# Kernel optimization log

Measured on AMD Instinct MI355X. Metric: run time of the kernel, lower is better.

Reference implementation:

```python
import jax, jax.numpy as jnp
import numpy as np

D_MODEL = 1024
BLOCK_SIZE = 2048


def setup_inputs() -> dict:
    key = jax.random.key(0)
    ks = jax.random.split(key, 9)
    B, T, C = 4, 2048, D_MODEL
    s = 1.0 / np.sqrt(C)
    return {
        "x": jax.random.normal(ks[0], (B, T, C), dtype=jnp.float32),
        "Wq": jax.random.normal(ks[1], (C, C), dtype=jnp.float32) * s,
        "bq": jnp.zeros((C,), dtype=jnp.float32),
        "Wk": jax.random.normal(ks[2], (C, C), dtype=jnp.float32) * s,
        "bk": jnp.zeros((C,), dtype=jnp.float32),
        "Wv": jax.random.normal(ks[3], (C, C), dtype=jnp.float32) * s,
        "bv": jnp.zeros((C,), dtype=jnp.float32),
        "Wo": jax.random.normal(ks[4], (C, C), dtype=jnp.float32) * s,
        "bo": jnp.zeros((C,), dtype=jnp.float32),
    }


def reference(x, Wq, bq, Wk, bk, Wv, bv, Wo, bo):
    B, T, C = x.shape
    q = x @ Wq + bq
    k = x @ Wk + bk
    v = x @ Wv + bv
    # NOTE: original module never splits heads; attention is over full d_model
    score = jnp.einsum("btc,bsc->bts", q, k) / jnp.sqrt(jnp.asarray(C, x.dtype))
    causal = jnp.tril(jnp.ones((T, T), dtype=bool))
    score = jnp.where(causal, score, jnp.asarray(-jnp.inf, x.dtype))
    probs = jax.nn.softmax(score, axis=-1)
    out = jnp.einsum("bts,bsc->btc", probs, v)
    return out @ Wo + bo
```

## Files before the change

### kernel.cpp

```cpp
#include <hip/hip_runtime.h>
#include <hip/hip_bf16.h>
#include <stdint.h>


typedef __attribute__((ext_vector_type(8))) __bf16 bf16x8;
typedef __attribute__((ext_vector_type(4))) __bf16 bf16x4;
typedef __attribute__((ext_vector_type(4))) float f32x4;

#define MFMA16(A, B, C) __builtin_amdgcn_mfma_f32_16x16x32_bf16(A, B, C, 0, 0, 0)
#define BAR() asm volatile("s_barrier" ::: "memory")

#define T_SEQ 2048
#define D_MOD 1024

static __device__ __forceinline__ void gload_lds16(const void* g, void* l) {
  __builtin_amdgcn_global_load_lds(
      (const __attribute__((address_space(1))) void*)g,
      (__attribute__((address_space(3))) void*)l, 16, 0, 0);
}

__global__ void cvt_bf16_kernel(const float* __restrict__ in,
                                __bf16* __restrict__ out, int n8) {
  int i = blockIdx.x * blockDim.x + threadIdx.x;
  if (i < n8) {
    const float4* p = (const float4*)(in + (size_t)i * 8);
    float4 a = p[0], b = p[1];
    bf16x8 o;
    o[0] = (__bf16)a.x; o[1] = (__bf16)a.y; o[2] = (__bf16)a.z; o[3] = (__bf16)a.w;
    o[4] = (__bf16)b.x; o[5] = (__bf16)b.y; o[6] = (__bf16)b.z; o[7] = (__bf16)b.w;
    *(bf16x8*)(out + (size_t)i * 8) = o;
  }
}

__global__ void transpose_cvt4_kernel(const float* __restrict__ Wq,
                                      const float* __restrict__ Wk,
                                      const float* __restrict__ Wv,
                                      const float* __restrict__ Wo,
                                      __bf16* __restrict__ Wqkvt,
                                      __bf16* __restrict__ Wot) {
  __shared__ float tile[32][33];
  const int z = blockIdx.z;
  const float* W = (z == 0) ? Wq : (z == 1) ? Wk : (z == 2) ? Wv : Wo;
  __bf16* Wt = (z < 3) ? (Wqkvt + (size_t)z * 1024 * 1024) : Wot;
  int tx = threadIdx.x, ty = threadIdx.y;
  int bx = blockIdx.x * 32, by = blockIdx.y * 32;
#pragma unroll
  for (int i = 0; i < 4; i++)
    tile[ty + 8 * i][tx] = W[(size_t)(by + ty + 8 * i) * D_MOD + bx + tx];
  __syncthreads();
#pragma unroll
  for (int i = 0; i < 4; i++)
    Wt[(size_t)(bx + ty + 8 * i) * D_MOD + by + tx] = (__bf16)tile[tx][ty + 8 * i];
}

__global__ __launch_bounds__(512, 2) void qkv384_kernel(
    const __bf16* __restrict__ A, const __bf16* __restrict__ Bt,
    const float* __restrict__ bq, const float* __restrict__ bk,
    const float* __restrict__ bv, __bf16* __restrict__ Qo,
    __bf16* __restrict__ Ko, __bf16* __restrict__ Vto) {
  constexpr int NT = 16;
  __shared__ __align__(16) char lds[131072];
#define ABUF(p) (lds + (p) * 16384)
#define BBUF(p) (lds + 32768 + (p) * 49152)

  const int tid = threadIdx.x;
  const int w = tid >> 6, l = tid & 63;
  const int wr = w >> 2, wc = w & 3;
  const int cpx = gridDim.x >> 3;
  const int swz = ((int)blockIdx.x & 7) * cpx + ((int)blockIdx.x >> 3);
  const int bm = (swz >> 3) * 128;
  const int bn = (swz & 7) * 384;

  const int cswz = (l & 3) ^ ((l >> 3) & 3);
  const int rlo = l & 15;
  const int xsw = (((l >> 4) ^ ((l >> 1) & 3)) << 4);

#define STAGE_A(t, p)                                                     \
  {                                                                       \
    const __bf16* g = A + (size_t)(bm + w * 16 + (l >> 2)) * 1024 +       \
                      (t) * 64 + cswz * 8;                                \
    char* d = ABUF(p) + w * 1024 + l * 16;                                \
    gload_lds16(g, d);                                                    \
    gload_lds16(g + 32, d + 8192);                                        \
  }
#define STAGE_B(t, p, gch)                                                \
  {                                                                       \
    const __bf16* g = Bt +                                                \
        (size_t)(bn + ((gch) * 8 + w) * 16 + (l >> 2)) * 1024 +           \
        (t) * 64 + cswz * 8;                                              \
    char* d = BBUF(p) + ((gch) * 8 + w) * 1024 + l * 16;                  \
    gload_lds16(g, d);                                                    \
    gload_lds16(g + 32, d + 24576);                                       \
  }
#define LDA_FRAG(p, i, kk)                                        \
  (*(const bf16x8*)(ABUF(p) + (kk) * 8192 +                       \
                    (wr * 64 + (i) * 16 + rlo) * 64 + xsw))
#define LDB_FRAG(p, gch, n, kk)                                   \
  (*(const bf16x8*)(BBUF(p) + (kk) * 24576 +                      \
                    (wc * 96 + (gch) * 32 + (n) * 16 + rlo) * 64 + xsw))

  f32x4 acc[4][6] = {};
  bf16x8 a_c[4][2], a_n[4][2], b0_c[2][2], b0_n[2][2], b1f[2][2], b2f[2][2];

  STAGE_A(0, 0);
  STAGE_B(0, 0, 0); STAGE_B(0, 0, 1); STAGE_B(0, 0, 2);
  STAGE_A(1, 1);
  STAGE_B(1, 1, 0); STAGE_B(1, 1, 1); STAGE_B(1, 1, 2);
  asm volatile("s_waitcnt vmcnt(8)" ::: "memory");
  BAR();
#pragma unroll
  for (int i = 0; i < 4; i++) {
    a_c[i][0] = LDA_FRAG(0, i, 0);
    a_c[i][1] = LDA_FRAG(0, i, 1);
  }
#pragma unroll
  for (int n = 0; n < 2; n++) {
    b0_c[n][0] = LDB_FRAG(0, 0, n, 0);
    b0_c[n][1] = LDB_FRAG(0, 0, n, 1);
  }

  for (int t = 0; t < NT; ++t) {
    const int p = t & 1;
#pragma unroll
    for (int n = 0; n < 2; n++) {
      b1f[n][0] = LDB_FRAG(p, 1, n, 0);
      b1f[n][1] = LDB_FRAG(p, 1, n, 1);
    }
    __builtin_amdgcn_s_setprio(1);
#pragma unroll
    for (int i = 0; i < 4; i++)
#pragma unroll
      for (int n = 0; n < 2; n++) {
        acc[i][n] = MFMA16(a_c[i][0], b0_c[n][0], acc[i][n]);
        acc[i][n] = MFMA16(a_c[i][1], b0_c[n][1], acc[i][n]);
      }
    __builtin_amdgcn_s_setprio(0);
    BAR();
#pragma unroll
    for (int n = 0; n < 2; n++) {
      b2f[n][0] = LDB_FRAG(p, 2, n, 0);
      b2f[n][1] = LDB_FRAG(p, 2, n, 1);
    }
    if (t + 2 < NT) STAGE_A(t + 2, p);
    __builtin_amdgcn_s_setprio(1);
#pragma unroll
    for (int i = 0; i < 4; i++)
#pragma unroll
      for (int n = 0; n < 2; n++) {
        acc[i][2 + n] = MFMA16(a_c[i][0], b1f[n][0], acc[i][2 + n]);
        acc[i][2 + n] = MFMA16(a_c[i][1], b1f[n][1], acc[i][2 + n]);
      }
    __builtin_amdgcn_s_setprio(0);
    if (t + 2 < NT) asm volatile("s_waitcnt vmcnt(2)" ::: "memory");
    else asm volatile("s_waitcnt vmcnt(0)" ::: "memory");
    BAR();
    if (t + 1 < NT) {
#pragma unroll
      for (int i = 0; i < 4; i++) {
        a_n[i][0] = LDA_FRAG(p ^ 1, i, 0);
        a_n[i][1] = LDA_FRAG(p ^ 1, i, 1);
      }
#pragma unroll
      for (int n = 0; n < 2; n++) {
        b0_n[n][0] = LDB_FRAG(p ^ 1, 0, n, 0);
        b0_n[n][1] = LDB_FRAG(p ^ 1, 0, n, 1);
      }
    }
    if (t + 2 < NT) {
      STAGE_B(t + 2, p, 0); STAGE_B(t + 2, p, 1); STAGE_B(t + 2, p, 2);
    }
    __builtin_amdgcn_s_setprio(1);
#pragma unroll
    for (int i = 0; i < 4; i++)
#pragma unroll
      for (int n = 0; n < 2; n++) {
        acc[i][4 + n] = MFMA16(a_c[i][0], b2f[n][0], acc[i][4 + n]);
        acc[i][4 + n] = MFMA16(a_c[i][1], b2f[n][1], acc[i][4 + n]);
      }
    __builtin_amdgcn_s_setprio(0);
    BAR();
    if (t + 1 < NT) {
#pragma unroll
      for (int i = 0; i < 4; i++) {
        a_c[i][0] = a_n[i][0];
        a_c[i][1] = a_n[i][1];
      }
#pragma unroll
      for (int n = 0; n < 2; n++) {
        b0_c[n][0] = b0_n[n][0];
        b0_c[n][1] = b0_n[n][1];
      }
    }
  }

  const int l4 = (l >> 4) * 4;
#pragma unroll
  for (int gch = 0; gch < 3; gch++)
#pragma unroll
    for (int n = 0; n < 2; n++) {
      const int cbase = bn + wc * 96 + gch * 32 + n * 16;
      const int seg = cbase >> 10;
      const int lcol = (cbase & 1023) + rlo;
      const int an = gch * 2 + n;
      if (seg < 2) {
        const float* bs = seg ? bk : bq;
        __bf16* os = seg ? Ko : Qo;
        const float bvv = bs[lcol];
#pragma unroll
        for (int i = 0; i < 4; i++) {
          const int rowb = bm + wr * 64 + i * 16 + l4;
#pragma unroll
          for (int r = 0; r < 4; r++)
            os[(size_t)(rowb + r) * D_MOD + lcol] =
                (__bf16)(acc[i][an][r] + bvv);
        }
      } else {
        const float bvv = bv[lcol];
#pragma unroll
        for (int i = 0; i < 4; i++) {
          const int rowb = bm + wr * 64 + i * 16 + l4;
          const int z = rowb >> 11, tt = rowb & 2047;
          bf16x4 pk;
#pragma unroll
          for (int r = 0; r < 4; r++) pk[r] = (__bf16)(acc[i][an][r] + bvv);
          *(bf16x4*)(Vto + (size_t)z * (D_MOD * T_SEQ) +
                     (size_t)lcol * T_SEQ + tt) = pk;
        }
      }
    }
#undef ABUF
#undef BBUF
#undef STAGE_A
#undef STAGE_B
#undef LDA_FRAG
#undef LDB_FRAG
}

template <int MG, int NG>
static __device__ __forceinline__ void mfma_quad(f32x4 (&acc)[8][4],
                                                 const bf16x8 (&aR)[4][2],
                                                 const bf16x8 (&bR)[2][2]) {
#pragma unroll
  for (int i = 0; i < 4; i++)
#pragma unroll
    for (int n = 0; n < 2; n++)
#pragma unroll
      for (int kk = 0; kk < 2; kk++)
        acc[MG * 4 + i][NG * 2 + n] =
            MFMA16(aR[i][kk], bR[n][kk], acc[MG * 4 + i][NG * 2 + n]);
}

__global__ __launch_bounds__(512, 2) void qk_kernel(
    const __bf16* __restrict__ A, const __bf16* __restrict__ Bt,
    float* __restrict__ So, size_t bsA, size_t bsB, size_t bsC) {
  constexpr int NT = 16;
  __shared__ __align__(16) char lds[131072];
#define ABUF(p, h) (lds + ((p) * 2 + (h)) * 16384)
#define BBUF(p, h) (lds + 65536 + ((p) * 2 + (h)) * 16384)

  const int tid = threadIdx.x;
  const int w = tid >> 6, l = tid & 63;
  const int wr = w >> 2, wc = w & 3;
  int x = (int)blockIdx.x;
  int ti = 0;
  while (x >= ti + 1) { x -= ti + 1; ++ti; }
  const int tj = x;
  const int bm = ti * 256, bn = tj * 256;
  const int z = blockIdx.z;
  A += (size_t)z * bsA;
  Bt += (size_t)z * bsB;

  const int grow = l >> 2;
  const int cswz = (l & 3) ^ ((l >> 3) & 3);
  const int rlo = l & 15;
  const int xsw = (((l >> 4) ^ ((l >> 1) & 3)) << 4);

#define STAGE_A(t, h)                                                       \
  {                                                                         \
    const __bf16* g = A + (size_t)(bm + (h) * 128 + w * 16 + grow) * 1024 + \
                      (t) * 64 + cswz * 8;                                  \
    char* d = ABUF((t) & 1, h) + w * 1024 + l * 16;                         \
    gload_lds16(g, d);                                                      \
    gload_lds16(g + 32, d + 8192);                                          \
  }
#define STAGE_B(t, h)                                                       \
  {                                                                         \
    const __bf16* g = Bt + (size_t)(bn + (h) * 128 + w * 16 + grow) * 1024 +\
                      (t) * 64 + cswz * 8;                                  \
    char* d = BBUF((t) & 1, h) + w * 1024 + l * 16;                         \
    gload_lds16(g, d);                                                      \
    gload_lds16(g + 32, d + 8192);                                          \
  }
#define LDA_FRAG(p, g, i, kk)                                     \
  (*(const bf16x8*)(ABUF(p, wr) + (kk) * 8192 +                   \
                    ((g) * 64 + (i) * 16 + rlo) * 64 + xsw))
#define LDB_FRAG(p, g, n, kk)                                     \
  (*(const bf16x8*)(BBUF(p, (wc >> 1)) + (kk) * 8192 +            \
                    ((wc & 1) * 64 + (g) * 32 + (n) * 16 + rlo) * 64 + xsw))

  f32x4 acc[8][4] = {};
  STAGE_A(0, 0); STAGE_A(0, 1);
  STAGE_B(0, 0); STAGE_B(0, 1);
  STAGE_A(1, 0); STAGE_A(1, 1);
  asm volatile("s_waitcnt vmcnt(4)" ::: "memory");
  BAR();

  for (int t = 0; t < NT; ++t) {
    const int p = t & 1;
    bf16x8 a[4][2], b[2][2];
#pragma unroll
    for (int i = 0; i < 4; i++) {
      a[i][0] = LDA_FRAG(p, 0, i, 0);
      a[i][1] = LDA_FRAG(p, 0, i, 1);
    }
#pragma unroll
    for (int n = 0; n < 2; n++) {
      b[n][0] = LDB_FRAG(p, 0, n, 0);
      b[n][1] = LDB_FRAG(p, 0, n, 1);
    }
    if (t + 1 < NT) STAGE_B(t + 1, 0);
    BAR();
    __builtin_amdgcn_s_setprio(1);
    mfma_quad<0, 0>(acc, a, b);
    __builtin_amdgcn_s_setprio(0);
    BAR();
    bf16x8 b2[2][2];
#pragma unroll
    for (int n = 0; n < 2; n++) {
      b2[n][0] = LDB_FRAG(p, 1, n, 0);
      b2[n][1] = LDB_FRAG(p, 1, n, 1);
    }
    if (t + 1 < NT) STAGE_B(t + 1, 1);
    BAR();
    __builtin_amdgcn_s_setprio(1);
    mfma_quad<0, 1>(acc, a, b2);
    __builtin_amdgcn_s_setprio(0);
    BAR();
#pragma unroll
    for (int i = 0; i < 4; i++) {
      a[i][0] = LDA_FRAG(p, 1, i, 0);
      a[i][1] = LDA_FRAG(p, 1, i, 1);
    }
    BAR();
    __builtin_amdgcn_s_setprio(1);
    mfma_quad<1, 1>(acc, a, b2);
    __builtin_amdgcn_s_setprio(0);
    BAR();
#pragma unroll
    for (int n = 0; n < 2; n++) {
      b[n][0] = LDB_FRAG(p, 0, n, 0);
      b[n][1] = LDB_FRAG(p, 0, n, 1);
    }
    if (t + 2 < NT) {
      STAGE_A(t + 2, 0); STAGE_A(t + 2, 1);
      BAR();
      __builtin_amdgcn_s_setprio(1);
      mfma_quad<1, 0>(acc, a, b);
      __builtin_amdgcn_s_setprio(0);
      asm volatile("s_waitcnt vmcnt(4)" ::: "memory");
      BAR();
    } else {
      BAR();
      __builtin_amdgcn_s_setprio(1);
      mfma_quad<1, 0>(acc, a, b);
      __builtin_amdgcn_s_setprio(0);
      asm volatile("s_waitcnt vmcnt(0)" ::: "memory");
      BAR();
    }
  }

  float* os = So + (size_t)z * bsC;
#pragma unroll
  for (int n4 = 0; n4 < 4; n4++) {
    int col = bn + wc * 64 + n4 * 16 + rlo;
#pragma unroll
    for (int mi = 0; mi < 8; mi++) {
      int rowb = bm + wr * 128 + mi * 16 + (l >> 4) * 4;
#pragma unroll
      for (int r = 0; r < 4; r++) {
        int row = rowb + r;
        float v = acc[mi][n4][r] * 0.03125f;
        if (col > row) v = -1e30f;
        os[(size_t)row * T_SEQ + col] = v;
      }
    }
  }
#undef ABUF
#undef BBUF
#undef STAGE_A
#undef STAGE_B
#undef LDA_FRAG
#undef LDB_FRAG
}

__global__ __launch_bounds__(512, 2) void pv_kernel(
    const __bf16* __restrict__ Ap, const __bf16* __restrict__ Btp,
    __bf16* __restrict__ Op, size_t bsA, size_t bsB, size_t bsC) {
  __shared__ __align__(16) char lds[98304];
#define ABUF(p3) (lds + (p3) * 16384)
#define BBUF(p3) (lds + 49152 + (p3) * 16384)

  const int tid = threadIdx.x;
  const int w = tid >> 6, l = tid & 63;
  const int wr = w >> 2, wc = w & 3;
  const int pid = (int)blockIdx.x >> 3;
  const int bn = ((int)blockIdx.x & 7) * 128;
  const int z = blockIdx.z;
  const __bf16* A = Ap + (size_t)z * bsA;
  const __bf16* Bt = Btp + (size_t)z * bsB;
  __bf16* O = Op + (size_t)z * bsC;

  const int grow = w * 16 + (l >> 2);
  const int cswz = (l & 3) ^ ((l >> 3) & 3);
  const int rlo = l & 15;
  const int xsw = (((l >> 4) ^ ((l >> 1) & 3)) << 4);

#define PSTAGE_A(t, p3)                                                      \
  {                                                                          \
    const __bf16* g = A + (size_t)(bm + grow) * 4096 + (t) * 64 + cswz * 8;  \
    char* d = ABUF(p3) + w * 1024 + l * 16;                                  \
    gload_lds16(g, d);                                                       \
    gload_lds16(g + 32, d + 8192);                                           \
  }
#define PSTAGE_B(t, p3)                                                      \
  {                                                                          \
    const __bf16* g = Bt + (size_t)(bn + grow) * 2048 + (t) * 64 + cswz * 8; \
    char* d = BBUF(p3) + w * 1024 + l * 16;                                  \
    gload_lds16(g, d);                                                       \
    gload_lds16(g + 32, d + 8192);                                           \
  }
#define PLDA(p3, i, kk)                                           \
  (*(const bf16x8*)(ABUF(p3) + (kk) * 8192 +                      \
                    (wr * 64 + (i) * 16 + rlo) * 64 + xsw))
#define PLDB(p3, n, kk)                                           \
  (*(const bf16x8*)(BBUF(p3) + (kk) * 8192 +                      \
                    (wc * 32 + (n) * 16 + rlo) * 64 + xsw))

#pragma unroll
  for (int seg = 0; seg < 2; ++seg) {
    const int i = seg ? (15 - pid) : pid;
    const int bm = i * 128;
    const int NT = (i + 1) * 2;
    f32x4 acc[4][2] = {};

    PSTAGE_A(0, 0); PSTAGE_B(0, 0);
    if (NT > 1) { PSTAGE_A(1, 1); PSTAGE_B(1, 1); }
    asm volatile("s_waitcnt vmcnt(4)" ::: "memory");
    BAR();

    int p = 0, pn2 = 2;
    for (int t = 0; t < NT; ++t) {
      bf16x8 af[4][2], bfv[2][2];
#pragma unroll
      for (int m = 0; m < 4; m++) {
        af[m][0] = PLDA(p, m, 0);
        af[m][1] = PLDA(p, m, 1);
      }
#pragma unroll
      for (int n = 0; n < 2; n++) {
        bfv[n][0] = PLDB(p, n, 0);
        bfv[n][1] = PLDB(p, n, 1);
      }
      if (t + 2 < NT) { PSTAGE_A(t + 2, pn2); PSTAGE_B(t + 2, pn2); }
      BAR();
      __builtin_amdgcn_s_setprio(1);
#pragma unroll
      for (int m = 0; m < 4; m++)
#pragma unroll
        for (int n = 0; n < 2; n++) {
          acc[m][n] = MFMA16(af[m][0], bfv[n][0], acc[m][n]);
          acc[m][n] = MFMA16(af[m][1], bfv[n][1], acc[m][n]);
        }
      __builtin_amdgcn_s_setprio(0);
      if (t + 2 < NT) asm volatile("s_waitcnt vmcnt(4)" ::: "memory");
      else asm volatile("s_waitcnt vmcnt(0)" ::: "memory");
      BAR();
      p = (p + 1 == 3) ? 0 : p + 1;
      pn2 = (pn2 + 1 == 3) ? 0 : pn2 + 1;
    }

#pragma unroll
    for (int n = 0; n < 2; n++) {
      int col = bn + wc * 32 + n * 16 + rlo;
#pragma unroll
      for (int m = 0; m < 4; m++) {
        int rowb = bm + wr * 64 + m * 16 + (l >> 4) * 4;
#pragma unroll
        for (int r = 0; r < 4; r++)
          O[(size_t)(rowb + r) * D_MOD + col] = (__bf16)acc[m][n][r];
      }
    }
    BAR();
  }
#undef ABUF
#undef BBUF
#undef PSTAGE_A
#undef PSTAGE_B
#undef PLDA
#undef PLDB
}

__global__ __launch_bounds__(512, 2) void oproj_kernel(
    const __bf16* __restrict__ A, const __bf16* __restrict__ Bt,
    const float* __restrict__ b0, float* __restrict__ o0) {
  constexpr int NT = 16;
  __shared__ __align__(16) char lds[147456];
#define ABUF(p3) (lds + (p3) * 16384)
#define BBUF(p3) (lds + 49152 + (p3) * 32768)

  const int tid = threadIdx.x;
  const int w = tid >> 6, l = tid & 63;
  const int wr = w >> 2, wc = w & 3;
  const int cpx = gridDim.x >> 3;
  const int swz = ((int)blockIdx.x & 7) * cpx + ((int)blockIdx.x >> 3);
  const int bm = (swz >> 2) * 128, bn = (swz & 3) * 256;

  const int grow = w * 16 + (l >> 2);
  const int cswz = (l & 3) ^ ((l >> 3) & 3);
  const int rlo = l & 15;
  const int xsw = (((l >> 4) ^ ((l >> 1) & 3)) << 4);

#define STAGE_A(t, p3)                                                       \
  {                                                                          \
    const __bf16* g = A + (size_t)(bm + grow) * 1024 + (t) * 64 + cswz * 8;  \
    char* d = ABUF(p3) + w * 1024 + l * 16;                                  \
    gload_lds16(g, d);                                                       \
    gload_lds16(g + 32, d + 8192);                                           \
  }
#define STAGE_B(t, p3)                                                       \
  {                                                                          \
    const __bf16* g = Bt + (size_t)(bn + grow) * 1024 + (t) * 64 + cswz * 8; \
    char* d = BBUF(p3) + w * 1024 + l * 16;                                  \
    gload_lds16(g, d);                                                       \
    gload_lds16(g + 32, d + 16384);                                          \
    const __bf16* g2 = g + (size_t)128 * 1024;                               \
    gload_lds16(g2, d + 8192);                                               \
    gload_lds16(g2 + 32, d + 8192 + 16384);                                  \
  }
#define LDA_FRAG(p3, i, kk)                                       \
  (*(const bf16x8*)(ABUF(p3) + (kk) * 8192 +                      \
                    (wr * 64 + (i) * 16 + rlo) * 64 + xsw))
#define LDB_FRAG(p3, n, kk)                                       \
  (*(const bf16x8*)(BBUF(p3) + (kk) * 16384 +                     \
                    (wc * 64 + (n) * 16 + rlo) * 64 + xsw))

  f32x4 acc[4][4] = {};
  STAGE_A(0, 0); STAGE_B(0, 0);
  STAGE_A(1, 1); STAGE_B(1, 1);
  asm volatile("s_waitcnt vmcnt(6)" ::: "memory");
  BAR();

  int p = 0, pn2 = 2;
  for (int t = 0; t < NT; ++t) {
    bf16x8 af[4][2], bf01[2][2], bf23[2][2];
#pragma unroll
    for (int i = 0; i < 4; i++) {
      af[i][0] = LDA_FRAG(p, i, 0);
      af[i][1] = LDA_FRAG(p, i, 1);
    }
#pragma unroll
    for (int n = 0; n < 2; n++) {
      bf01[n][0] = LDB_FRAG(p, n, 0);
      bf01[n][1] = LDB_FRAG(p, n, 1);
    }
    if (t + 2 < NT) STAGE_A(t + 2, pn2);
    BAR();
    __builtin_amdgcn_s_setprio(1);
#pragma unroll
    for (int i = 0; i < 4; i++)
#pragma unroll
      for (int n = 0; n < 2; n++) {
        acc[i][n] = MFMA16(af[i][0], bf01[n][0], acc[i][n]);
        acc[i][n] = MFMA16(af[i][1], bf01[n][1], acc[i][n]);
      }
    __builtin_amdgcn_s_setprio(0);
    BAR();
#pragma unroll
    for (int n = 0; n < 2; n++) {
      bf23[n][0] = LDB_FRAG(p, n + 2, 0);
      bf23[n][1] = LDB_FRAG(p, n + 2, 1);
    }
    if (t + 2 < NT) STAGE_B(t + 2, pn2);
    BAR();
    __builtin_amdgcn_s_setprio(1);
#pragma unroll
    for (int i = 0; i < 4; i++)
#pragma unroll
      for (int n = 0; n < 2; n++) {
        acc[i][n + 2] = MFMA16(af[i][0], bf23[n][0], acc[i][n + 2]);
        acc[i][n + 2] = MFMA16(af[i][1], bf23[n][1], acc[i][n + 2]);
      }
    __builtin_amdgcn_s_setprio(0);
    if (t + 2 < NT) {
      asm volatile("s_waitcnt vmcnt(6)" ::: "memory");
    } else {
      asm volatile("s_waitcnt vmcnt(0)" ::: "memory");
    }
    BAR();
    p = (p + 1 == 3) ? 0 : p + 1;
    pn2 = (pn2 + 1 == 3) ? 0 : pn2 + 1;
  }

#pragma unroll
  for (int n = 0; n < 4; n++) {
    int col = bn + wc * 64 + n * 16 + rlo;
    float bvv = b0[col];
#pragma unroll
    for (int m = 0; m < 4; m++) {
      int rowb = bm + wr * 64 + m * 16 + (l >> 4) * 4;
#pragma unroll
      for (int r = 0; r < 4; r++)
        o0[(size_t)(rowb + r) * D_MOD + col] = acc[m][n][r] + bvv;
    }
  }
#undef ABUF
#undef BBUF
#undef STAGE_A
#undef STAGE_B
#undef LDA_FRAG
#undef LDB_FRAG
}

__global__ __launch_bounds__(256) void softmax_kernel(float* __restrict__ S,
                                                      size_t bstride) {
  const int t = blockIdx.x, b = blockIdx.y;
  float* Srow = S + (size_t)b * bstride + (size_t)t * T_SEQ;
  __bf16* Prow = (__bf16*)Srow;
  const int L = ((t + 1) + 127) & ~127;
  const int tid = threadIdx.x;
  const int base = tid * 8;
  const bool act = base < L;
  float v[8];
  float m = -1e30f;
  if (act) {
    float4 a = *(const float4*)(Srow + base);
    float4 c = *(const float4*)(Srow + base + 4);
    v[0] = a.x; v[1] = a.y; v[2] = a.z; v[3] = a.w;
    v[4] = c.x; v[5] = c.y; v[6] = c.z; v[7] = c.w;
#pragma unroll
    for (int j = 0; j < 8; j++) m = fmaxf(m, v[j]);
  }
#pragma unroll
  for (int off = 1; off < 64; off <<= 1) m = fmaxf(m, __shfl_xor(m, off));
  __shared__ float redm[4], reds[4];
  const int wave = tid >> 6, lane = tid & 63;
  if (lane == 0) redm[wave] = m;
  __syncthreads();
  m = fmaxf(fmaxf(redm[0], redm[1]), fmaxf(redm[2], redm[3]));
  float p[8];
  float s = 0.f;
  if (act) {
#pragma unroll
    for (int j = 0; j < 8; j++) {
      p[j] = __expf(v[j] - m);
      s += p[j];
    }
  }
#pragma unroll
  for (int off = 1; off < 64; off <<= 1) s += __shfl_xor(s, off);
  if (lane == 0) reds[wave] = s;
  __syncthreads();
  const float inv = 1.0f / (reds[0] + reds[1] + reds[2] + reds[3]);
  if (act) {
    bf16x8 o;
#pragma unroll
    for (int j = 0; j < 8; j++) o[j] = (__bf16)(p[j] * inv);
    *(bf16x8*)(Prow + base) = o;
  }
}

extern "C" void kernel_launch(void* const* d_in, const int* in_sizes, int n_in,
                              void* d_out, int out_size, void* d_ws,
                              size_t ws_size, hipStream_t stream) {
  const float* x = (const float*)d_in[0];
  const float* Wq = (const float*)d_in[1];
  const float* bq = (const float*)d_in[2];
  const float* Wk = (const float*)d_in[3];
  const float* bk = (const float*)d_in[4];
  const float* Wv = (const float*)d_in[5];
  const float* bv = (const float*)d_in[6];
  const float* Wo = (const float*)d_in[7];
  const float* bo = (const float*)d_in[8];

  char* ws = (char*)d_ws;
  const size_t MB = 1u << 20;
  const size_t TC = (size_t)T_SEQ * D_MOD;
  const size_t TT = (size_t)T_SEQ * T_SEQ;
  __bf16* xb    = (__bf16*)(ws);
  __bf16* Wqkvt = (__bf16*)(ws + 16 * MB);
  __bf16* Wot   = (__bf16*)(ws + 22 * MB);
  __bf16* Qb    = (__bf16*)(ws + 24 * MB);
  __bf16* Kb    = (__bf16*)(ws + 40 * MB);
  __bf16* Vtb   = (__bf16*)(ws + 56 * MB);

  cvt_bf16_kernel<<<4096, 256, 0, stream>>>(x, xb, 8192 * D_MOD / 8);
  transpose_cvt4_kernel<<<dim3(32, 32, 4), dim3(32, 8), 0, stream>>>(
      Wq, Wk, Wv, Wo, Wqkvt, Wot);
  qkv384_kernel<<<512, 512, 0, stream>>>(xb, Wqkvt, bq, bk, bv, Qb, Kb, Vtb);

  const bool batched = ws_size >= 137 * MB;
  if (batched) {
    float* S = (float*)(ws + 72 * MB);
    __bf16* AO = Qb;
    qk_kernel<<<dim3(36, 1, 4), 512, 0, stream>>>(Qb, Kb, S, TC, TC, TT);
    softmax_kernel<<<dim3(T_SEQ, 4), 256, 0, stream>>>(S, TT);
    pv_kernel<<<dim3(64, 1, 4), 512, 0, stream>>>((const __bf16*)S, Vtb, AO,
                                                  TT * 2, TC, TC);
    oproj_kernel<<<256, 512, 0, stream>>>(AO, Wot, bo, (float*)d_out);
  } else {
    float* S = (float*)(ws);
    __bf16* AO = Qb;
    for (int b = 0; b < 4; ++b) {
      qk_kernel<<<dim3(36, 1, 1), 512, 0, stream>>>(Qb + b * TC, Kb + b * TC,
                                                    S, 0, 0, 0);
      softmax_kernel<<<dim3(T_SEQ, 1), 256, 0, stream>>>(S, 0);
      pv_kernel<<<dim3(64, 1, 1), 512, 0, stream>>>(
          (const __bf16*)S, Vtb + b * TC, AO + b * TC, 0, 0, 0);
    }
    oproj_kernel<<<256, 512, 0, stream>>>(AO, Wot, bo, (float*)d_out);
  }
}
```

Measured before the change: 170.4 us.

## Replace 128x384 QKV GEMM tile with 128x256 tile and simpler pipeline

Replaces the QKV projection kernel's 128x384 output tile (K-step 64, 128KB LDS) with a 128x256 tile (K-step 32, 48KB LDS), launched on 768 blocks instead of 512. The main loop becomes a simpler double-buffered loop with one fragment load phase and one MFMA phase per step, and the staggered register prefetch is dropped. The aim is to cut LDS use so more blocks fit per CU and to balance work across CUs. The trade-off is less data reuse per tile, twice as many K iterations, and two barriers per step with less overlap of loads and math.

```diff
diff --git a/kernel.cpp b/kernel.cpp
--- a/kernel.cpp
+++ b/kernel.cpp
@@ -53,187 +53,116 @@
     Wt[(size_t)(bx + ty + 8 * i) * D_MOD + by + tx] = (__bf16)tile[tx][ty + 8 * i];
 }
 
-__global__ __launch_bounds__(512, 2) void qkv384_kernel(
+__global__ __launch_bounds__(512, 2) void qkv256_kernel(
     const __bf16* __restrict__ A, const __bf16* __restrict__ Bt,
     const float* __restrict__ bq, const float* __restrict__ bk,
     const float* __restrict__ bv, __bf16* __restrict__ Qo,
     __bf16* __restrict__ Ko, __bf16* __restrict__ Vto) {
-  constexpr int NT = 16;
-  __shared__ __align__(16) char lds[131072];
-#define ABUF(p) (lds + (p) * 16384)
-#define BBUF(p) (lds + 32768 + (p) * 49152)
+  constexpr int NT = 32;
+  __shared__ __align__(16) char lds[49152];
+#define ABUF(p) (lds + (p) * 8192)
+#define BBUF(p) (lds + 16384 + (p) * 16384)
 
   const int tid = threadIdx.x;
   const int w = tid >> 6, l = tid & 63;
   const int wr = w >> 2, wc = w & 3;
   const int cpx = gridDim.x >> 3;
   const int swz = ((int)blockIdx.x & 7) * cpx + ((int)blockIdx.x >> 3);
-  const int bm = (swz >> 3) * 128;
-  const int bn = (swz & 7) * 384;
+  const int bm = (swz / 12) * 128;
+  const int bn = (swz % 12) * 256;
 
   const int cswz = (l & 3) ^ ((l >> 3) & 3);
   const int rlo = l & 15;
   const int xsw = (((l >> 4) ^ ((l >> 1) & 3)) << 4);
-
-#define STAGE_A(t, p)                                                     \
-  {                                                                       \
-    const __bf16* g = A + (size_t)(bm + w * 16 + (l >> 2)) * 1024 +       \
-                      (t) * 64 + cswz * 8;                                \
-    char* d = ABUF(p) + w * 1024 + l * 16;                                \
-    gload_lds16(g, d);                                                    \
-    gload_lds16(g + 32, d + 8192);                                        \
-  }
-#define STAGE_B(t, p, gch)                                                \
-  {                                                                       \
-    const __bf16* g = Bt +                                                \
-        (size_t)(bn + ((gch) * 8 + w) * 16 + (l >> 2)) * 1024 +           \
-        (t) * 64 + cswz * 8;                                              \
-    char* d = BBUF(p) + ((gch) * 8 + w) * 1024 + l * 16;                  \
-    gload_lds16(g, d);                                                    \
-    gload_lds16(g + 32, d + 24576);                                       \
-  }
-#define LDA_FRAG(p, i, kk)                                        \
-  (*(const bf16x8*)(ABUF(p) + (kk) * 8192 +                       \
-                    (wr * 64 + (i) * 16 + rlo) * 64 + xsw))
-#define LDB_FRAG(p, gch, n, kk)                                   \
-  (*(const bf16x8*)(BBUF(p) + (kk) * 24576 +                      \
-                    (wc * 96 + (gch) * 32 + (n) * 16 + rlo) * 64 + xsw))
-
-  f32x4 acc[4][6] = {};
-  bf16x8 a_c[4][2], a_n[4][2], b0_c[2][2], b0_n[2][2], b1f[2][2], b2f[2][2];
-
-  STAGE_A(0, 0);
-  STAGE_B(0, 0, 0); STAGE_B(0, 0, 1); STAGE_B(0, 0, 2);
-  STAGE_A(1, 1);
-  STAGE_B(1, 1, 0); STAGE_B(1, 1, 1); STAGE_B(1, 1, 2);
-  asm volatile("s_waitcnt vmcnt(8)" ::: "memory");
+  const int srow = w * 16 + (l >> 2);
+
+#define STAGE_A(t, p)                                                  \
+  {                                                                    \
+    const __bf16* g = A + (size_t)(bm + srow) * 1024 + (t) * 32 +      \
+                      cswz * 8;                                        \
+    gload_lds16(g, ABUF(p) + w * 1024 + l * 16);                       \
+  }
+#define STAGE_B(t, p)                                                  \
+  {                                                                    \
+    const __bf16* g0 = Bt + (size_t)(bn + srow) * 1024 + (t) * 32 +    \
+                       cswz * 8;                                       \
+    char* d = BBUF(p) + w * 1024 + l * 16;                             \
+    gload_lds16(g0, d);                                                \
+    gload_lds16(g0 + (size_t)128 * 1024, d + 8192);                    \
+  }
+
+  f32x4 acc[4][4] = {};
+  STAGE_A(0, 0); STAGE_B(0, 0);
+  STAGE_A(1, 1); STAGE_B(1, 1);
+  asm volatile("s_waitcnt vmcnt(3)" ::: "memory");
   BAR();
-#pragma unroll
-  for (int i = 0; i < 4; i++) {
-    a_c[i][0] = LDA_FRAG(0, i, 0);
-    a_c[i][1] = LDA_FRAG(0, i, 1);
-  }
-#pragma unroll
-  for (int n = 0; n < 2; n++) {
-    b0_c[n][0] = LDB_FRAG(0, 0, n, 0);
-    b0_c[n][1] = LDB_FRAG(0, 0, n, 1);
-  }
 
   for (int t = 0; t < NT; ++t) {
     const int p = t & 1;
-#pragma unroll
-    for (int n = 0; n < 2; n++) {
-      b1f[n][0] = LDB_FRAG(p, 1, n, 0);
-      b1f[n][1] = LDB_FRAG(p, 1, n, 1);
+    bf16x8 af[4], bf[4];
+#pragma unroll
+    for (int i = 0; i < 4; i++)
+      af[i] = *(const bf16x8*)(ABUF(p) + (wr * 64 + i * 16 + rlo) * 64 + xsw);
+#pragma unroll
+    for (int n = 0; n < 4; n++)
+      bf[n] = *(const bf16x8*)(BBUF(p) + (wc * 64 + n * 16 + rlo) * 64 + xsw);
+    asm volatile("s_waitcnt lgkmcnt(0)" ::: "memory");
+    BAR();
+    if (t + 2 < NT) {
+      STAGE_A(t + 2, p);
+      STAGE_B(t + 2, p);
     }
     __builtin_amdgcn_s_setprio(1);
 #pragma unroll
     for (int i = 0; i < 4; i++)
 #pragma unroll
-      for (int n = 0; n < 2; n++) {
-        acc[i][n] = MFMA16(a_c[i][0], b0_c[n][0], acc[i][n]);
-        acc[i][n] = MFMA16(a_c[i][1], b0_c[n][1], acc[i][n]);
-      }
+      for (int n = 0; n < 4; n++)
+        acc[i][n] = MFMA16(af[i], bf[n], acc[i][n]);
     __builtin_amdgcn_s_setprio(0);
-    BAR();
-#pragma unroll
-    for (int n = 0; n < 2; n++) {
-      b2f[n][0] = LDB_FRAG(p, 2, n, 0);
-      b2f[n][1] = LDB_FRAG(p, 2, n, 1);
-    }
-    if (t + 2 < NT) STAGE_A(t + 2, p);
-    __builtin_amdgcn_s_setprio(1);
-#pragma unroll
-    for (int i = 0; i < 4; i++)
-#pragma unroll
-      for (int n = 0; n < 2; n++) {
-        acc[i][2 + n] = MFMA16(a_c[i][0], b1f[n][0], acc[i][2 + n]);
-        acc[i][2 + n] = MFMA16(a_c[i][1], b1f[n][1], acc[i][2 + n]);
-      }
-    __builtin_amdgcn_s_setprio(0);
-    if (t + 2 < NT) asm volatile("s_waitcnt vmcnt(2)" ::: "memory");
+    if (t + 2 < NT) asm volatile("s_waitcnt vmcnt(3)" ::: "memory");
     else asm volatile("s_waitcnt vmcnt(0)" ::: "memory");
     BAR();
-    if (t + 1 < NT) {
-#pragma unroll
-      for (int i = 0; i < 4; i++) {
-        a_n[i][0] = LDA_FRAG(p ^ 1, i, 0);
-        a_n[i][1] = LDA_FRAG(p ^ 1, i, 1);
-      }
-#pragma unroll
-      for (int n = 0; n < 2; n++) {
-        b0_n[n][0] = LDB_FRAG(p ^ 1, 0, n, 0);
-        b0_n[n][1] = LDB_FRAG(p ^ 1, 0, n, 1);
-      }
-    }
-    if (t + 2 < NT) {
-      STAGE_B(t + 2, p, 0); STAGE_B(t + 2, p, 1); STAGE_B(t + 2, p, 2);
-    }
-    __builtin_amdgcn_s_setprio(1);
-#pragma unroll
-    for (int i = 0; i < 4; i++)
-#pragma unroll
-      for (int n = 0; n < 2; n++) {
-        acc[i][4 + n] = MFMA16(a_c[i][0], b2f[n][0], acc[i][4 + n]);
-        acc[i][4 + n] = MFMA16(a_c[i][1], b2f[n][1], acc[i][4 + n]);
-      }
-    __builtin_amdgcn_s_setprio(0);
-    BAR();
-    if (t + 1 < NT) {
-#pragma unroll
-      for (int i = 0; i < 4; i++) {
-        a_c[i][0] = a_n[i][0];
-        a_c[i][1] = a_n[i][1];
-      }
-#pragma unroll
-      for (int n = 0; n < 2; n++) {
-        b0_c[n][0] = b0_n[n][0];
-        b0_c[n][1] = b0_n[n][1];
-      }
-    }
   }
 
   const int l4 = (l >> 4) * 4;
-#pragma unroll
-  for (int gch = 0; gch < 3; gch++)
-#pragma unroll
-    for (int n = 0; n < 2; n++) {
-      const int cbase = bn + wc * 96 + gch * 32 + n * 16;
-      const int seg = cbase >> 10;
-      const int lcol = (cbase & 1023) + rlo;
-      const int an = gch * 2 + n;
-      if (seg < 2) {
-        const float* bs = seg ? bk : bq;
-        __bf16* os = seg ? Ko : Qo;
-        const float bvv = bs[lcol];
-#pragma unroll
-        for (int i = 0; i < 4; i++) {
-          const int rowb = bm + wr * 64 + i * 16 + l4;
-#pragma unroll
-          for (int r = 0; r < 4; r++)
-            os[(size_t)(rowb + r) * D_MOD + lcol] =
-                (__bf16)(acc[i][an][r] + bvv);
-        }
-      } else {
-        const float bvv = bv[lcol];
-#pragma unroll
-        for (int i = 0; i < 4; i++) {
-          const int rowb = bm + wr * 64 + i * 16 + l4;
-          const int z = rowb >> 11, tt = rowb & 2047;
-          bf16x4 pk;
-#pragma unroll
-          for (int r = 0; r < 4; r++) pk[r] = (__bf16)(acc[i][an][r] + bvv);
-          *(bf16x4*)(Vto + (size_t)z * (D_MOD * T_SEQ) +
-                     (size_t)lcol * T_SEQ + tt) = pk;
-        }
-      }
-    }
+  const int seg = bn >> 10;
+  const int bnl = bn & 1023;
+  if (seg < 2) {
+    const float* bs = seg ? bk : bq;
+    __bf16* os = seg ? Ko : Qo;
+#pragma unroll
+    for (int n4 = 0; n4 < 4; n4++) {
+      int col = bnl + wc * 64 + n4 * 16 + rlo;
+      float bvv = bs[col];
+#pragma unroll
+      for (int m = 0; m < 4; m++) {
+        int rowb = bm + wr * 64 + m * 16 + l4;
+#pragma unroll
+        for (int r = 0; r < 4; r++)
+          os[(size_t)(rowb + r) * D_MOD + col] = (__bf16)(acc[m][n4][r] + bvv);
+      }
+    }
+  } else {
+#pragma unroll
+    for (int n4 = 0; n4 < 4; n4++) {
+      int lcol = bnl + wc * 64 + n4 * 16 + rlo;
+      float bvv = bv[lcol];
+#pragma unroll
+      for (int m = 0; m < 4; m++) {
+        int rowb = bm + wr * 64 + m * 16 + l4;
+        int zz = rowb >> 11, tt = rowb & 2047;
+        bf16x4 pk;
+#pragma unroll
+        for (int r = 0; r < 4; r++) pk[r] = (__bf16)(acc[m][n4][r] + bvv);
+        *(bf16x4*)(Vto + (size_t)zz * (D_MOD * T_SEQ) + (size_t)lcol * T_SEQ +
+                   tt) = pk;
+      }
+    }
+  }
 #undef ABUF
 #undef BBUF
 #undef STAGE_A
 #undef STAGE_B
-#undef LDA_FRAG
-#undef LDB_FRAG
 }
 
 template <int MG, int NG>
@@ -696,7 +625,7 @@
   cvt_bf16_kernel<<<4096, 256, 0, stream>>>(x, xb, 8192 * D_MOD / 8);
   transpose_cvt4_kernel<<<dim3(32, 32, 4), dim3(32, 8), 0, stream>>>(
       Wq, Wk, Wv, Wo, Wqkvt, Wot);
-  qkv384_kernel<<<512, 512, 0, stream>>>(xb, Wqkvt, bq, bk, bv, Qb, Kb, Vtb);
+  qkv256_kernel<<<768, 512, 0, stream>>>(xb, Wqkvt, bq, bk, bv, Qb, Kb, Vtb);
 
   const bool batched = ws_size >= 137 * MB;
   if (batched) {
```

Result: no change. 171.5 us (+0.6%).
